# Kernel tuning notes

Measured on AMD Instinct MI355X. Metric: run time of the kernel, lower is better.

Reference implementation:

```python
import jax, jax.numpy as jnp
import numpy as np

N = 100_000      # nodes
E = 400_000      # edges
NPERM = 100_000  # local receptive-field subgraphs
L = 16           # lrp_length
H = 64           # hid_dim
NLAYERS = 4
G = 1024         # graphs in the batch
P = NPERM * L    # permutation rows (must be NPERM * L)


def _spmm(row, col, val, mat, m):
    # COO sparse [m, n] @ dense [n, d]  (torch_sparse.spmm equivalent)
    return jax.ops.segment_sum(val[:, None] * mat[col], row, num_segments=m)


def setup_inputs() -> dict:
    key = jax.random.key(0)
    ks = jax.random.split(key, 16)
    inp = {}
    inp["node_feat"] = jax.random.normal(ks[0], (N, 28), jnp.float32)
    inp["degs"] = jax.random.uniform(ks[1], (N,), jnp.float32) * 8.0
    inp["batch"] = jnp.sort(jax.random.randint(ks[2], (N,), 0, G)).astype(jnp.int32)
    # node -> perm-length permutation matrix (one nonzero per perm row)
    inp["n2p_row"] = jnp.arange(P, dtype=jnp.int32)
    inp["n2p_col"] = jax.random.randint(ks[3], (P,), 0, N, dtype=jnp.int32)
    inp["n2p_val"] = jnp.ones((P,), jnp.float32)
    # edge -> perm-length permutation matrix
    inp["e2p_row"] = jnp.arange(P, dtype=jnp.int32)
    inp["e2p_col"] = jax.random.randint(ks[4], (P,), 0, E, dtype=jnp.int32)
    inp["e2p_val"] = jnp.ones((P,), jnp.float32)
    # pooling matrix: subgraph row -> root node, shape [N, NPERM]
    inp["pool_row"] = jax.random.randint(ks[5], (NPERM,), 0, N, dtype=jnp.int32)
    inp["pool_col"] = jnp.arange(NPERM, dtype=jnp.int32)
    inp["pool_val"] = jax.random.uniform(ks[6], (NPERM,), jnp.float32)
    # parameters
    inp["atom_W"] = jax.random.normal(ks[7], (28, H), jnp.float32) * 0.1
    inp["atom_b"] = jnp.zeros((H,), jnp.float32)
    inp["edge_W"] = jax.random.normal(ks[8], (1, H), jnp.float32) * 0.1
    inp["edge_b"] = jnp.zeros((H,), jnp.float32)
    inp["W_lrp"] = jax.random.normal(ks[9], (NLAYERS, H, H, L), jnp.float32) * 0.03
    inp["b_lrp"] = jnp.zeros((NLAYERS, H), jnp.float32)
    inp["dn0_W"] = jax.random.normal(ks[10], (NLAYERS, 1, 2 * H), jnp.float32) * 0.2
    inp["dn0_b"] = jnp.zeros((NLAYERS, 2 * H), jnp.float32)
    inp["dn1_W"] = jax.random.normal(ks[11], (NLAYERS, 2 * H, H), jnp.float32) * 0.1
    inp["dn1_b"] = jnp.zeros((NLAYERS, H), jnp.float32)
    return inp


def reference(node_feat, degs, batch,
              n2p_row, n2p_col, n2p_val,
              e2p_row, e2p_col, e2p_val,
              pool_row, pool_col, pool_val,
              atom_W, atom_b, edge_W, edge_b,
              W_lrp, b_lrp, dn0_W, dn0_b, dn1_W, dn1_b):
    x = node_feat @ atom_W + atom_b                       # atom_encoder  [N, H]
    # all edge features are 1 -> edge_encoder gives identical rows
    efeat = jnp.ones((E, 1), node_feat.dtype) @ edge_W + edge_b  # [E, H]
    for i in range(NLAYERS):
        # gather nodes + edges into perm-length layout   [P, H]
        perm = _spmm(n2p_row, n2p_col, n2p_val, x, P) \
             + _spmm(e2p_row, e2p_col, e2p_val, efeat, P)
        # transpose(0,1).view(H,-1,L).permute(1,2,0) == reshape(NPERM, L, H)
        t = perm.reshape(NPERM, L, H)
        # einsum('dab,bca->dc') with weights [H_in, H_out, L]
        h = jax.nn.relu(jnp.einsum('plh,hcl->pc', t, W_lrp[i]) + b_lrp[i])  # [NPERM, H]
        pooled = _spmm(pool_row, pool_col, pool_val, h, N)  # [N, H]
        hid = jax.nn.relu(degs[:, None] @ dn0_W[i] + dn0_b[i])  # [N, 2H]
        factor = hid @ dn1_W[i] + dn1_b[i]                      # [N, H]
        x = pooled * factor
    # global mean pool over graphs
    sums = jax.ops.segment_sum(x, batch, num_segments=G)
    cnts = jax.ops.segment_sum(jnp.ones((x.shape[0],), x.dtype), batch, num_segments=G)
    return sums / jnp.maximum(cnts, 1.0)[:, None]
```

## Files before the change

### kernel.cpp

```cpp
#include <hip/hip_runtime.h>

typedef __attribute__((ext_vector_type(8))) short bf16x8;
typedef __attribute__((ext_vector_type(4))) float f32x4;

#define N_NODES   100000
#define NPERM_    100000
#define L_        16
#define G_        1024
#define CAP_      20
#define OVF_MAX   4096

__device__ inline unsigned short f32_to_bf16(float f) {
    unsigned u = __float_as_uint(f);
    unsigned r = (u + 0x7fff + ((u >> 16) & 1)) >> 16;
    return (unsigned short)r;
}
__device__ inline float bflo(unsigned u) { return __uint_as_float(u << 16); }
__device__ inline float bfhi(unsigned u) { return __uint_as_float(u & 0xffff0000u); }
__device__ inline unsigned pk2(float a, float b) {
    return (unsigned)f32_to_bf16(a) | ((unsigned)f32_to_bf16(b) << 16);
}

__global__ __launch_bounds__(256) void k_prep_w(const float* __restrict__ W,
                                                unsigned short* __restrict__ Wh,
                                                unsigned short* __restrict__ Wl) {
    int o = blockIdx.x * 256 + threadIdx.x;
    int k = o & 63, c = (o >> 6) & 63, l = (o >> 12) & 15, i = o >> 16;
    float f = W[(((i * 64 + k) * 64) + c) * 16 + l];
    unsigned short hh = f32_to_bf16(f);
    float fl = f - __uint_as_float(((unsigned)hh) << 16);
    Wh[o] = hh;
    Wl[o] = f32_to_bf16(fl);
}

__global__ __launch_bounds__(256) void k_prep_factor(const float* __restrict__ dn0_W,
                                                     const float* __restrict__ dn0_b,
                                                     const float* __restrict__ dn1_W,
                                                     const float* __restrict__ dn1_b,
                                                     float* __restrict__ tab,
                                                     float* __restrict__ thr) {
    int i     = blockIdx.x;
    int chunk = blockIdx.y;
    int tid   = threadIdx.x;
    __shared__ float A[128], B[128], ts[128], tv[128];
    __shared__ float W1l[128 * 64];
    if (tid < 128) { A[tid] = dn0_W[i * 128 + tid]; B[tid] = dn0_b[i * 128 + tid]; }
    {
        const float4* src = (const float4*)(dn1_W + (size_t)i * 8192);
        float4*       dst = (float4*)W1l;
        for (int t = tid; t < 2048; t += 256) dst[t] = src[t];
    }
    __syncthreads();
    if (tid < 128) {
        float a = A[tid], b = B[tid];
        float tj = -b / a;
        if (a == 0.f || !(tj > 0.f)) tj = 1e30f;
        tv[tid] = tj;
    }
    __syncthreads();
    if (tid < 128) {
        float tj = tv[tid];
        int rank = 0;
        for (int j = 0; j < 128; ++j) {
            float o = tv[j];
            rank += (o < tj) || (o == tj && j < tid);
        }
        ts[rank] = tj;
    }
    __syncthreads();
    if (chunk == 0 && tid < 128) thr[i * 128 + tid] = ts[tid];
    int s0 = chunk * 17;
    int s1 = min(s0 + 17, 129);
    float* tb = tab + (size_t)i * 129 * 128;
    for (int item = s0 * 64 + tid; item < s1 * 64; item += 256) {
        int s = item >> 6;
        int c = item & 63;
        float lo = (s == 0) ? 0.f : ts[s - 1];
        float hi = (s == 128) ? 1e30f : ts[s];
        float g;
        if (lo > 1e29f)       g = 1e29f;
        else if (hi > 1e29f)  g = lo + 1.f;
        else                  g = 0.5f * (lo + hi);
        float alpha = 0.f, beta = dn1_b[i * 64 + c];
        for (int j = 0; j < 128; ++j) {
            if (fmaf(g, A[j], B[j]) > 0.f) {
                float w1 = W1l[j * 64 + c];
                alpha = fmaf(A[j], w1, alpha);
                beta  = fmaf(B[j], w1, beta);
            }
        }
        tb[s * 128 + c * 2 + 0] = alpha;
        tb[s * 128 + c * 2 + 1] = beta;
    }
}

__global__ __launch_bounds__(256) void k_atom(const float* __restrict__ feat,
                                              const float* __restrict__ W,
                                              const float* __restrict__ b,
                                              unsigned short* __restrict__ xb) {
    __shared__ float Wlds[28 * 64];
    __shared__ float blds[64];
    int tid = threadIdx.x;
    for (int t = tid; t < 28 * 64; t += 256) Wlds[t] = W[t];
    if (tid < 64) blds[tid] = b[tid];
    __syncthreads();
    int n = blockIdx.x * 4 + (tid >> 6);
    int c = tid & 63;
    if (n >= N_NODES) return;
    const float* fr = feat + n * 28;
    float acc = blds[c];
#pragma unroll
    for (int j = 0; j < 28; ++j) acc = fmaf(fr[j], Wlds[j * 64 + c], acc);
    xb[n * 64 + c] = f32_to_bf16(acc);
}

__global__ __launch_bounds__(256) void k_bucket(const int* __restrict__ prow,
                                                int* __restrict__ cntn,
                                                int* __restrict__ bucket,
                                                int* __restrict__ ovf,
                                                int* __restrict__ ovfc) {
    int d = blockIdx.x * 256 + threadIdx.x;
    if (d >= NPERM_) return;
    int n = prow[d];
    int s = atomicAdd(cntn + n, 1);
    if (s < CAP_) bucket[n * CAP_ + s] = d;
    else { int o = atomicAdd(ovfc, 1); if (o < OVF_MAX) ovf[o] = d; }
}

__global__ __launch_bounds__(256, 4) void k_lrp(const unsigned short* __restrict__ xbuf,
                                                const int*   __restrict__ n2p_col,
                                                const float* __restrict__ n2p_val,
                                                const float* __restrict__ e2p_val,
                                                const float* __restrict__ edge_W,
                                                const float* __restrict__ edge_b,
                                                const unsigned short* __restrict__ Wth,
                                                const unsigned short* __restrict__ Wtl,
                                                const float* __restrict__ bl,
                                                float* __restrict__ hout) {
    __shared__ unsigned short Tb[128][72];
    __shared__ unsigned short Wh[64][72];
    __shared__ unsigned short Wo[64][72];
    __shared__ float efs[64];
    int tid = threadIdx.x;
    int lane = tid & 63;
    int w = tid >> 6;
    int d0 = blockIdx.x * 128;
    int dl = tid >> 1;
    int kq = tid & 1;
    int wc = tid >> 2;
    int wk = (tid & 3) * 16;
    int dg = d0 + dl;
    int dsafe = (dg < NPERM_) ? dg : 0;
    size_t pbase = (size_t)dsafe * 16;

    if (tid < 64) efs[tid] = edge_W[tid] + edge_b[tid];

    f32x4 acc[2][4];
#pragma unroll
    for (int aa = 0; aa < 2; ++aa)
#pragma unroll
        for (int cb = 0; cb < 4; ++cb) acc[aa][cb] = (f32x4)0.f;

    uint4 xvA[4], xvB[4], wvh0, wvh1, wvl0, wvl1;
    int   colN  = n2p_col[pbase + 2];
    int   colN2 = n2p_col[pbase + 3];
    float vnN   = n2p_val[pbase + 0];
    float veN   = e2p_val[pbase + 0];
    {
        int c0 = n2p_col[pbase + 0];
        int c1 = n2p_col[pbase + 1];
        const uint4* xr0 = (const uint4*)(xbuf + (size_t)c0 * 64 + kq * 32);
#pragma unroll
        for (int j = 0; j < 4; ++j) xvA[j] = xr0[j];
        const uint4* xr1 = (const uint4*)(xbuf + (size_t)c1 * 64 + kq * 32);
#pragma unroll
        for (int j = 0; j < 4; ++j) xvB[j] = xr1[j];
        const uint4* whr = (const uint4*)(Wth + wc * 64 + wk);
        wvh0 = whr[0]; wvh1 = whr[1];
        const uint4* wlr = (const uint4*)(Wtl + wc * 64 + wk);
        wvl0 = wlr[0]; wvl1 = wlr[1];
    }
    __syncthreads();

#define LRP_PHASE(LVAL, XV)                                                      \
    {                                                                            \
        const int l = (LVAL);                                                    \
        float vn = vnN, ve = veN;                                                \
        __syncthreads();                                                         \
        _Pragma("unroll")                                                        \
        for (int j = 0; j < 4; ++j) {                                            \
            uint4 v = XV[j];                                                     \
            int kb = kq * 32 + j * 8;                                            \
            float4 ea = *(const float4*)&efs[kb];                                \
            float4 eb = *(const float4*)&efs[kb + 4];                            \
            float t0 = fmaf(vn, bflo(v.x), ve * ea.x);                           \
            float t1 = fmaf(vn, bfhi(v.x), ve * ea.y);                           \
            float t2 = fmaf(vn, bflo(v.y), ve * ea.z);                           \
            float t3 = fmaf(vn, bfhi(v.y), ve * ea.w);                           \
            float t4 = fmaf(vn, bflo(v.z), ve * eb.x);                           \
            float t5 = fmaf(vn, bfhi(v.z), ve * eb.y);                           \
            float t6 = fmaf(vn, bflo(v.w), ve * eb.z);                           \
            float t7 = fmaf(vn, bfhi(v.w), ve * eb.w);                           \
            uint4 ow;                                                            \
            ow.x = pk2(t0, t1); ow.y = pk2(t2, t3);                              \
            ow.z = pk2(t4, t5); ow.w = pk2(t6, t7);                              \
            *(uint4*)&Tb[dl][kb] = ow;                                           \
        }                                                                        \
        *(uint4*)&Wh[wc][wk]     = wvh0;                                         \
        *(uint4*)&Wh[wc][wk + 8] = wvh1;                                         \
        *(uint4*)&Wo[wc][wk]     = wvl0;                                         \
        *(uint4*)&Wo[wc][wk + 8] = wvl1;                                         \
        __syncthreads();                                                         \
        if (l < 15) {                                                            \
            const uint4* whr = (const uint4*)(Wth + (l + 1) * 4096 + wc * 64 + wk); \
            wvh0 = whr[0]; wvh1 = whr[1];                                        \
            const uint4* wlr = (const uint4*)(Wtl + (l + 1) * 4096 + wc * 64 + wk); \
            wvl0 = wlr[0]; wvl1 = wlr[1];                                        \
            vnN = n2p_val[pbase + l + 1];                                        \
            veN = e2p_val[pbase + l + 1];                                        \
        }                                                                        \
        if (l < 14) {           \
            const uint4* xr = (const uint4*)(xbuf + (size_t)colN * 64 + kq * 32);\
            _Pragma("unroll")                                                    \
            for (int j = 0; j < 4; ++j) XV[j] = xr[j];                           \
            colN = colN2;                                                        \
            if (l < 12) colN2 = n2p_col[pbase + l + 4];                          \
        }                                                                        \
        {                                                                        \
            int r = lane & 15, q = lane >> 4;                                    \
            _Pragma("unroll")                                                    \
            for (int s = 0; s < 2; ++s) {                                        \
                int ko = s * 32 + q * 8;                                         \
                bf16x8 a0 = *(const bf16x8*)&Tb[w * 32 + r][ko];                 \
                bf16x8 a1 = *(const bf16x8*)&Tb[w * 32 + 16 + r][ko];            \
                _Pragma("unroll")                                                \
                for (int cb = 0; cb < 4; ++cb) {                                 \
                    bf16x8 bh = *(const bf16x8*)&Wh[cb * 16 + r][ko];            \
                    bf16x8 bo = *(const bf16x8*)&Wo[cb * 16 + r][ko];            \
                    acc[0][cb] = __builtin_amdgcn_mfma_f32_16x16x32_bf16(a0, bh, acc[0][cb], 0, 0, 0); \
                    acc[0][cb] = __builtin_amdgcn_mfma_f32_16x16x32_bf16(a0, bo, acc[0][cb], 0, 0, 0); \
                    acc[1][cb] = __builtin_amdgcn_mfma_f32_16x16x32_bf16(a1, bh, acc[1][cb], 0, 0, 0); \
                    acc[1][cb] = __builtin_amdgcn_mfma_f32_16x16x32_bf16(a1, bo, acc[1][cb], 0, 0, 0); \
                }                                                                \
            }                                                                    \
        }                                                                        \
    }

#pragma unroll 1
    for (int lp = 0; lp < 8; ++lp) {
        LRP_PHASE(2 * lp,     xvA)
        LRP_PHASE(2 * lp + 1, xvB)
    }
#undef LRP_PHASE

    __syncthreads();
    {
        int r = lane & 15, q = lane >> 4;
        float* F = (float*)(&Tb[0][0]) + w * 1024;
#pragma unroll
        for (int aa = 0; aa < 2; ++aa) {
#pragma unroll
            for (int cb = 0; cb < 4; ++cb) {
                float bias = bl[cb * 16 + r];
#pragma unroll
                for (int reg = 0; reg < 4; ++reg)
                    F[(q * 4 + reg) * 64 + cb * 16 + r] = fmaxf(acc[aa][cb][reg] + bias, 0.f);
            }
#pragma unroll
            for (int ii = 0; ii < 4; ++ii) {
                int idx = lane + ii * 64;
                float4 v = ((const float4*)F)[idx];
                int R = d0 + w * 32 + aa * 16 + (idx >> 4);
                if (R < NPERM_)
                    *(float4*)(hout + (size_t)R * 64 + (idx & 15) * 4) = v;
            }
        }
    }
}

__global__ __launch_bounds__(256) void k_pool_seg(const float* __restrict__ h,
                                                  const int*   __restrict__ cntn,
                                                  const int*   __restrict__ bucket,
                                                  const int*   __restrict__ ovf,
                                                  const int*   __restrict__ ovfc,
                                                  const int*   __restrict__ prow,
                                                  const float* __restrict__ pval,
                                                  const float* __restrict__ degs,
                                                  const float* __restrict__ tab,
                                                  const float* __restrict__ thr,
                                                  float* __restrict__ x,
                                                  unsigned short* __restrict__ xbo,
                                                  int last) {
    __shared__ float thrl[128];
    int tid = threadIdx.x;
    if (tid < 128) thrl[tid] = thr[tid];
    __syncthreads();
    int n  = blockIdx.x * 16 + (tid >> 4);
    int c4 = (tid & 15) * 4;
    if (n >= N_NODES) return;
    float dgv = degs[n];
    int seg = 0;
    if (thrl[63]       < dgv) seg = 64;
    if (thrl[seg + 31] < dgv) seg += 32;
    if (thrl[seg + 15] < dgv) seg += 16;
    if (thrl[seg + 7]  < dgv) seg += 8;
    if (thrl[seg + 3]  < dgv) seg += 4;
    if (thrl[seg + 1]  < dgv) seg += 2;
    if (thrl[seg]      < dgv) seg += 1;
    float4 p = make_float4(0.f, 0.f, 0.f, 0.f);
    int cn = min(cntn[n], CAP_);
    for (int j = 0; j < cn; ++j) {
        int   d  = bucket[n * CAP_ + j];
        float pv = pval[d];
        float4 hv = *(const float4*)(h + (size_t)d * 64 + c4);
        p.x = fmaf(pv, hv.x, p.x);
        p.y = fmaf(pv, hv.y, p.y);
        p.z = fmaf(pv, hv.z, p.z);
        p.w = fmaf(pv, hv.w, p.w);
    }
    int novf = *ovfc;
    if (novf > 0) {
        int ne = novf < OVF_MAX ? novf : OVF_MAX;
        for (int e = 0; e < ne; ++e) {
            int d = ovf[e];
            if (prow[d] == n) {
                float pv = pval[d];
                float4 hv = *(const float4*)(h + (size_t)d * 64 + c4);
                p.x = fmaf(pv, hv.x, p.x);
                p.y = fmaf(pv, hv.y, p.y);
                p.z = fmaf(pv, hv.z, p.z);
                p.w = fmaf(pv, hv.w, p.w);
            }
        }
    }
    const float4* tf = (const float4*)(tab + (size_t)(seg * 64 + c4) * 2);
    float4 t0 = tf[0], t1 = tf[1];
    float4 xo;
    xo.x = p.x * fmaf(t0.x, dgv, t0.y);
    xo.y = p.y * fmaf(t0.z, dgv, t0.w);
    xo.z = p.z * fmaf(t1.x, dgv, t1.y);
    xo.w = p.w * fmaf(t1.z, dgv, t1.w);
    if (last) {
        *(float4*)(x + (size_t)n * 64 + c4) = xo;
    } else {
        ushort4 s;
        s.x = f32_to_bf16(xo.x); s.y = f32_to_bf16(xo.y);
        s.z = f32_to_bf16(xo.z); s.w = f32_to_bf16(xo.w);
        *(ushort4*)(xbo + (size_t)n * 64 + c4) = s;
    }
}

__global__ __launch_bounds__(256) void k_gpool(const float* __restrict__ x,
                                               const int* __restrict__ batch,
                                               float* __restrict__ out,
                                               float* __restrict__ cnt) {
    int wave = (blockIdx.x * 256 + threadIdx.x) >> 6;
    int lane = threadIdx.x & 63;
    int n0 = wave * 64;
    if (n0 >= N_NODES) return;
    int n1 = min(n0 + 64, N_NODES);
    int g = batch[n0];
    float s = 0.f, c = 0.f;
    for (int n = n0; n < n1; ++n) {
        int gn = batch[n];
        if (gn != g) {
            atomicAdd(out + (size_t)g * 64 + lane, s);
            if (lane == 0) atomicAdd(cnt + g, c);
            s = 0.f; c = 0.f; g = gn;
        }
        s += x[(size_t)n * 64 + lane];
        c += 1.f;
    }
    atomicAdd(out + (size_t)g * 64 + lane, s);
    if (lane == 0) atomicAdd(cnt + g, c);
}

__global__ __launch_bounds__(256) void k_gdiv(float* __restrict__ out,
                                              const float* __restrict__ cnt) {
    int idx = blockIdx.x * 256 + threadIdx.x;
    if (idx >= G_ * 64) return;
    out[idx] /= fmaxf(cnt[idx >> 6], 1.f);
}

extern "C" void kernel_launch(void* const* d_in, const int* in_sizes, int n_in,
                              void* d_out, int out_size, void* d_ws, size_t ws_size,
                              hipStream_t stream) {
    const float* node_feat = (const float*)d_in[0];
    const float* degs      = (const float*)d_in[1];
    const int*   batch     = (const int*)  d_in[2];
    const int*   n2p_col   = (const int*)  d_in[4];
    const float* n2p_val   = (const float*)d_in[5];
    const float* e2p_val   = (const float*)d_in[8];
    const int*   pool_row  = (const int*)  d_in[9];
    const float* pool_val  = (const float*)d_in[11];
    const float* atom_W    = (const float*)d_in[12];
    const float* atom_b    = (const float*)d_in[13];
    const float* edge_W    = (const float*)d_in[14];
    const float* edge_b    = (const float*)d_in[15];
    const float* W_lrp     = (const float*)d_in[16];
    const float* b_lrp     = (const float*)d_in[17];
    const float* dn0_W     = (const float*)d_in[18];
    const float* dn0_b     = (const float*)d_in[19];
    const float* dn1_W     = (const float*)d_in[20];
    const float* dn1_b     = (const float*)d_in[21];

    char* ws = (char*)d_ws;
    float*          h      = (float*)         (ws);
    unsigned short* xb     = (unsigned short*)(ws + 25600000);
    unsigned short* Wth    = (unsigned short*)(ws + 38400000);
    unsigned short* Wtl    = (unsigned short*)(ws + 38924288);
    int*            bucket = (int*)           (ws + 39448576);
    int*            cntn   = (int*)           (ws + 47448576);
    int*            ovf    = (int*)           (ws + 47848576);
    int*            ovfc   = (int*)           (ws + 47864960);
    float*          tab    = (float*)         (ws + 47865088);
    float*          thr    = (float*)         (ws + 48129280);
    float*          cntg   = (float*)         (ws + 48131328);
    float*          x      = (float*)         (ws + 48135424);

    hipLaunchKernelGGL(k_prep_w, dim3(1024), dim3(256), 0, stream, W_lrp, Wth, Wtl);
    hipLaunchKernelGGL(k_prep_factor, dim3(4, 8), dim3(256), 0, stream,
                       dn0_W, dn0_b, dn1_W, dn1_b, tab, thr);
    hipLaunchKernelGGL(k_atom, dim3(25000), dim3(256), 0, stream,
                       node_feat, atom_W, atom_b, xb);
    hipMemsetAsync(cntn, 0, 400000, stream);
    hipMemsetAsync(ovfc, 0, 128, stream);
    hipLaunchKernelGGL(k_bucket, dim3(391), dim3(256), 0, stream,
                       pool_row, cntn, bucket, ovf, ovfc);
    for (int i = 0; i < 4; ++i) {
        hipLaunchKernelGGL(k_lrp, dim3(782), dim3(256), 0, stream,
                           xb, n2p_col, n2p_val, e2p_val, edge_W, edge_b,
                           Wth + (size_t)i * 65536, Wtl + (size_t)i * 65536,
                           b_lrp + i * 64, h);
        hipLaunchKernelGGL(k_pool_seg, dim3(6250), dim3(256), 0, stream,
                           h, cntn, bucket, ovf, ovfc, pool_row, pool_val,
                           degs, tab + (size_t)i * 129 * 128, thr + i * 128,
                           x, xb, (i == 3) ? 1 : 0);
    }
    hipMemsetAsync(d_out, 0, (size_t)G_ * 64 * 4, stream);
    hipMemsetAsync(cntg, 0, G_ * 4, stream);
    hipLaunchKernelGGL(k_gpool, dim3(391), dim3(256), 0, stream,
                       x, batch, (float*)d_out, cntg);
    hipLaunchKernelGGL(k_gdiv, dim3(256), dim3(256), 0, stream,
                       (float*)d_out, cntg);
}
```

Measured before the change: 596.9 us.

## Store LRP output in bf16 and halve rows per k_lrp block

The LRP kernel now writes its relu output h as bf16 instead of fp32, and the pooling kernel reads and upconverts bf16, which halves the traffic of the intermediate h buffer. Each block now handles 64 subgraphs instead of 128, with four threads per row gathering x, so the grid doubles and the launch bound rises to 5 blocks per CU for more occupancy. The two memsets are merged into one covering cntn and ovfc, and the workspace is repacked. In exchange, h loses precision to bf16 rounding, and each block reloads the weights for half as many rows, which lowers weight reuse.

```diff
diff --git a/kernel.cpp b/kernel.cpp
--- a/kernel.cpp
+++ b/kernel.cpp
@@ -17,6 +17,7 @@
 }
 __device__ inline float bflo(unsigned u) { return __uint_as_float(u << 16); }
 __device__ inline float bfhi(unsigned u) { return __uint_as_float(u & 0xffff0000u); }
+__device__ inline float bfup(unsigned short s) { return __uint_as_float((unsigned)s << 16); }
 __device__ inline unsigned pk2(float a, float b) {
     return (unsigned)f32_to_bf16(a) | ((unsigned)f32_to_bf16(b) << 16);
 }
@@ -127,7 +128,7 @@
     else { int o = atomicAdd(ovfc, 1); if (o < OVF_MAX) ovf[o] = d; }
 }
 
-__global__ __launch_bounds__(256, 4) void k_lrp(const unsigned short* __restrict__ xbuf,
+__global__ __launch_bounds__(256, 5) void k_lrp(const unsigned short* __restrict__ xbuf,
                                                 const int*   __restrict__ n2p_col,
                                                 const float* __restrict__ n2p_val,
                                                 const float* __restrict__ e2p_val,
@@ -136,17 +137,17 @@
                                                 const unsigned short* __restrict__ Wth,
                                                 const unsigned short* __restrict__ Wtl,
                                                 const float* __restrict__ bl,
-                                                float* __restrict__ hout) {
-    __shared__ unsigned short Tb[128][72];
+                                                unsigned short* __restrict__ hout) {
+    __shared__ unsigned short Tb[64][72];
     __shared__ unsigned short Wh[64][72];
     __shared__ unsigned short Wo[64][72];
     __shared__ float efs[64];
     int tid = threadIdx.x;
     int lane = tid & 63;
     int w = tid >> 6;
-    int d0 = blockIdx.x * 128;
-    int dl = tid >> 1;
-    int kq = tid & 1;
+    int d0 = blockIdx.x * 64;
+    int dl = tid >> 2;
+    int kq = tid & 3;
     int wc = tid >> 2;
     int wk = (tid & 3) * 16;
     int dg = d0 + dl;
@@ -155,13 +156,11 @@
 
     if (tid < 64) efs[tid] = edge_W[tid] + edge_b[tid];
 
-    f32x4 acc[2][4];
+    f32x4 acc[4];
 #pragma unroll
-    for (int aa = 0; aa < 2; ++aa)
-#pragma unroll
-        for (int cb = 0; cb < 4; ++cb) acc[aa][cb] = (f32x4)0.f;
-
-    uint4 xvA[4], xvB[4], wvh0, wvh1, wvl0, wvl1;
+    for (int cb = 0; cb < 4; ++cb) acc[cb] = (f32x4)0.f;
+
+    uint4 xvA[2], xvB[2], wvh0, wvh1, wvl0, wvl1;
     int   colN  = n2p_col[pbase + 2];
     int   colN2 = n2p_col[pbase + 3];
     float vnN   = n2p_val[pbase + 0];
@@ -169,12 +168,10 @@
     {
         int c0 = n2p_col[pbase + 0];
         int c1 = n2p_col[pbase + 1];
-        const uint4* xr0 = (const uint4*)(xbuf + (size_t)c0 * 64 + kq * 32);
-#pragma unroll
-        for (int j = 0; j < 4; ++j) xvA[j] = xr0[j];
-        const uint4* xr1 = (const uint4*)(xbuf + (size_t)c1 * 64 + kq * 32);
-#pragma unroll
-        for (int j = 0; j < 4; ++j) xvB[j] = xr1[j];
+        const uint4* xr0 = (const uint4*)(xbuf + (size_t)c0 * 64 + kq * 16);
+        xvA[0] = xr0[0]; xvA[1] = xr0[1];
+        const uint4* xr1 = (const uint4*)(xbuf + (size_t)c1 * 64 + kq * 16);
+        xvB[0] = xr1[0]; xvB[1] = xr1[1];
         const uint4* whr = (const uint4*)(Wth + wc * 64 + wk);
         wvh0 = whr[0]; wvh1 = whr[1];
         const uint4* wlr = (const uint4*)(Wtl + wc * 64 + wk);
@@ -188,9 +185,9 @@
         float vn = vnN, ve = veN;                                                \
         __syncthreads();                                                         \
         _Pragma("unroll")                                                        \
-        for (int j = 0; j < 4; ++j) {                                            \
+        for (int j = 0; j < 2; ++j) {                                            \
             uint4 v = XV[j];                                                     \
-            int kb = kq * 32 + j * 8;                                            \
+            int kb = kq * 16 + j * 8;                                            \
             float4 ea = *(const float4*)&efs[kb];                                \
             float4 eb = *(const float4*)&efs[kb + 4];                            \
             float t0 = fmaf(vn, bflo(v.x), ve * ea.x);                           \
@@ -220,9 +217,8 @@
             veN = e2p_val[pbase + l + 1];                                        \
         }                                                                        \
         if (l < 14) {           \
-            const uint4* xr = (const uint4*)(xbuf + (size_t)colN * 64 + kq * 32);\
-            _Pragma("unroll")                                                    \
-            for (int j = 0; j < 4; ++j) XV[j] = xr[j];                           \
+            const uint4* xr = (const uint4*)(xbuf + (size_t)colN * 64 + kq * 16);\
+            XV[0] = xr[0]; XV[1] = xr[1];                                        \
             colN = colN2;                                                        \
             if (l < 12) colN2 = n2p_col[pbase + l + 4];                          \
         }                                                                        \
@@ -231,16 +227,13 @@
             _Pragma("unroll")                                                    \
             for (int s = 0; s < 2; ++s) {                                        \
                 int ko = s * 32 + q * 8;                                         \
-                bf16x8 a0 = *(const bf16x8*)&Tb[w * 32 + r][ko];                 \
-                bf16x8 a1 = *(const bf16x8*)&Tb[w * 32 + 16 + r][ko];            \
+                bf16x8 a0 = *(const bf16x8*)&Tb[w * 16 + r][ko];                 \
                 _Pragma("unroll")                                                \
                 for (int cb = 0; cb < 4; ++cb) {                                 \
                     bf16x8 bh = *(const bf16x8*)&Wh[cb * 16 + r][ko];            \
                     bf16x8 bo = *(const bf16x8*)&Wo[cb * 16 + r][ko];            \
-                    acc[0][cb] = __builtin_amdgcn_mfma_f32_16x16x32_bf16(a0, bh, acc[0][cb], 0, 0, 0); \
-                    acc[0][cb] = __builtin_amdgcn_mfma_f32_16x16x32_bf16(a0, bo, acc[0][cb], 0, 0, 0); \
-                    acc[1][cb] = __builtin_amdgcn_mfma_f32_16x16x32_bf16(a1, bh, acc[1][cb], 0, 0, 0); \
-                    acc[1][cb] = __builtin_amdgcn_mfma_f32_16x16x32_bf16(a1, bo, acc[1][cb], 0, 0, 0); \
+                    acc[cb] = __builtin_amdgcn_mfma_f32_16x16x32_bf16(a0, bh, acc[cb], 0, 0, 0); \
+                    acc[cb] = __builtin_amdgcn_mfma_f32_16x16x32_bf16(a0, bo, acc[cb], 0, 0, 0); \
                 }                                                                \
             }                                                                    \
         }                                                                        \
@@ -256,29 +249,27 @@
     __syncthreads();
     {
         int r = lane & 15, q = lane >> 4;
-        float* F = (float*)(&Tb[0][0]) + w * 1024;
+        unsigned short* F = &Tb[0][0] + w * 1024;
 #pragma unroll
-        for (int aa = 0; aa < 2; ++aa) {
+        for (int cb = 0; cb < 4; ++cb) {
+            float bias = bl[cb * 16 + r];
 #pragma unroll
-            for (int cb = 0; cb < 4; ++cb) {
-                float bias = bl[cb * 16 + r];
+            for (int reg = 0; reg < 4; ++reg)
+                F[(q * 4 + reg) * 64 + cb * 16 + r] =
+                    f32_to_bf16(fmaxf(acc[cb][reg] + bias, 0.f));
+        }
 #pragma unroll
-                for (int reg = 0; reg < 4; ++reg)
-                    F[(q * 4 + reg) * 64 + cb * 16 + r] = fmaxf(acc[aa][cb][reg] + bias, 0.f);
-            }
-#pragma unroll
-            for (int ii = 0; ii < 4; ++ii) {
-                int idx = lane + ii * 64;
-                float4 v = ((const float4*)F)[idx];
-                int R = d0 + w * 32 + aa * 16 + (idx >> 4);
-                if (R < NPERM_)
-                    *(float4*)(hout + (size_t)R * 64 + (idx & 15) * 4) = v;
-            }
-        }
-    }
-}
-
-__global__ __launch_bounds__(256) void k_pool_seg(const float* __restrict__ h,
+        for (int ii = 0; ii < 2; ++ii) {
+            int idx = lane + ii * 64;
+            uint4 v = ((const uint4*)F)[idx];
+            int R = d0 + w * 16 + (idx >> 3);
+            if (R < NPERM_)
+                *(uint4*)(hout + (size_t)R * 64 + (idx & 7) * 8) = v;
+        }
+    }
+}
+
+__global__ __launch_bounds__(256) void k_pool_seg(const unsigned short* __restrict__ h,
                                                   const int*   __restrict__ cntn,
                                                   const int*   __restrict__ bucket,
                                                   const int*   __restrict__ ovf,
@@ -312,11 +303,11 @@
     for (int j = 0; j < cn; ++j) {
         int   d  = bucket[n * CAP_ + j];
         float pv = pval[d];
-        float4 hv = *(const float4*)(h + (size_t)d * 64 + c4);
-        p.x = fmaf(pv, hv.x, p.x);
-        p.y = fmaf(pv, hv.y, p.y);
-        p.z = fmaf(pv, hv.z, p.z);
-        p.w = fmaf(pv, hv.w, p.w);
+        ushort4 hv = *(const ushort4*)(h + (size_t)d * 64 + c4);
+        p.x = fmaf(pv, bfup(hv.x), p.x);
+        p.y = fmaf(pv, bfup(hv.y), p.y);
+        p.z = fmaf(pv, bfup(hv.z), p.z);
+        p.w = fmaf(pv, bfup(hv.w), p.w);
     }
     int novf = *ovfc;
     if (novf > 0) {
@@ -325,11 +316,11 @@
             int d = ovf[e];
             if (prow[d] == n) {
                 float pv = pval[d];
-                float4 hv = *(const float4*)(h + (size_t)d * 64 + c4);
-                p.x = fmaf(pv, hv.x, p.x);
-                p.y = fmaf(pv, hv.y, p.y);
-                p.z = fmaf(pv, hv.z, p.z);
-                p.w = fmaf(pv, hv.w, p.w);
+                ushort4 hv = *(const ushort4*)(h + (size_t)d * 64 + c4);
+                p.x = fmaf(pv, bfup(hv.x), p.x);
+                p.y = fmaf(pv, bfup(hv.y), p.y);
+                p.z = fmaf(pv, bfup(hv.z), p.z);
+                p.w = fmaf(pv, bfup(hv.w), p.w);
             }
         }
     }
@@ -405,30 +396,29 @@
     const float* dn1_b     = (const float*)d_in[21];
 
     char* ws = (char*)d_ws;
-    float*          h      = (float*)         (ws);
-    unsigned short* xb     = (unsigned short*)(ws + 25600000);
-    unsigned short* Wth    = (unsigned short*)(ws + 38400000);
-    unsigned short* Wtl    = (unsigned short*)(ws + 38924288);
-    int*            bucket = (int*)           (ws + 39448576);
-    int*            cntn   = (int*)           (ws + 47448576);
-    int*            ovf    = (int*)           (ws + 47848576);
-    int*            ovfc   = (int*)           (ws + 47864960);
-    float*          tab    = (float*)         (ws + 47865088);
-    float*          thr    = (float*)         (ws + 48129280);
-    float*          cntg   = (float*)         (ws + 48131328);
-    float*          x      = (float*)         (ws + 48135424);
+    unsigned short* h      = (unsigned short*)(ws);
+    unsigned short* xb     = (unsigned short*)(ws + 12800000);
+    unsigned short* Wth    = (unsigned short*)(ws + 25600000);
+    unsigned short* Wtl    = (unsigned short*)(ws + 26124288);
+    int*            bucket = (int*)           (ws + 26648576);
+    int*            cntn   = (int*)           (ws + 34648576);
+    int*            ovf    = (int*)           (ws + 35048576);
+    int*            ovfc   = (int*)           (ws + 35064960);
+    float*          tab    = (float*)         (ws + 35065088);
+    float*          thr    = (float*)         (ws + 35329280);
+    float*          cntg   = (float*)         (ws + 35331328);
+    float*          x      = (float*)         (ws + 35335424);
 
     hipLaunchKernelGGL(k_prep_w, dim3(1024), dim3(256), 0, stream, W_lrp, Wth, Wtl);
     hipLaunchKernelGGL(k_prep_factor, dim3(4, 8), dim3(256), 0, stream,
                        dn0_W, dn0_b, dn1_W, dn1_b, tab, thr);
     hipLaunchKernelGGL(k_atom, dim3(25000), dim3(256), 0, stream,
                        node_feat, atom_W, atom_b, xb);
-    hipMemsetAsync(cntn, 0, 400000, stream);
-    hipMemsetAsync(ovfc, 0, 128, stream);
+    hipMemsetAsync(cntn, 0, 416512, stream);
     hipLaunchKernelGGL(k_bucket, dim3(391), dim3(256), 0, stream,
                        pool_row, cntn, bucket, ovf, ovfc);
     for (int i = 0; i < 4; ++i) {
-        hipLaunchKernelGGL(k_lrp, dim3(782), dim3(256), 0, stream,
+        hipLaunchKernelGGL(k_lrp, dim3(1563), dim3(256), 0, stream,
                            xb, n2p_col, n2p_val, e2p_val, edge_W, edge_b,
                            Wth + (size_t)i * 65536, Wtl + (size_t)i * 65536,
                            b_lrp + i * 64, h);
```

Result: no change. 596.6 us (-0.1%).
